# Optimization experiments

Hardware: AMD Instinct MI355X
Metric: run time of the kernel (lower is better)

The kernel has to match this reference:

```python
import jax, jax.numpy as jnp
import numpy as np

# Sizes matching init_kwargs: r=2, J=3 -> K = 1 + (r-1)*J = 4 framelet operators
N, FEAT, K, NNZ = 20000, 64, 4, 320000
NU, GAMMA, J = 2.0, 1.0, 3  # nu, gamma_0 (gamma never updated on this code path)


def setup_inputs() -> dict:
    key = jax.random.key(0)
    ks = jax.random.split(key, 6)
    F = jax.random.normal(ks[0], (N, FEAT), dtype=jnp.float32)
    w_rows = jax.random.randint(ks[1], (K, NNZ), 0, N, dtype=jnp.int32)
    w_cols = jax.random.randint(ks[2], (K, NNZ), 0, N, dtype=jnp.int32)
    # scale ~1/avg_degree so the 14-step fixed-point iteration is contractive/stable
    w_vals = jax.random.normal(ks[3], (K, NNZ), dtype=jnp.float32) / 16.0
    d = jax.random.uniform(ks[4], (N,), dtype=jnp.float32)
    mask = jax.random.uniform(ks[5], (N, 1), dtype=jnp.float32)
    return {"F": F, "w_rows": w_rows, "w_cols": w_cols, "w_vals": w_vals,
            "d": d, "mask": mask, "thres_iter": 15}


def _spmm(rows, cols, vals, X):
    # sparse [N,N] @ dense [N,FEAT] via gather + segment-sum scatter
    return jax.ops.segment_sum(vals[:, None] * X[cols], rows, num_segments=N)


_spmm_shared = jax.vmap(_spmm, in_axes=(0, 0, 0, None))  # K operators, one dense X
_spmm_each = jax.vmap(_spmm, in_axes=(0, 0, 0, 0))       # K operators, K dense Xs


def _soft(x, thr):  # elementwise soft-thresholding: relu(x-t) - relu(-x-t)
    return jax.nn.relu(x - thr) - jax.nn.relu(-x - thr)


def reference(F, w_rows, w_cols, w_vals, d, mask, thres_iter):
    # nu_jl = [0] + [nu / 4^i for i in range(J)]
    nu = jnp.asarray([0.0] + [NU / (4.0 ** i) for i in range(J)], dtype=jnp.float32)  # [K]
    thr = (nu / GAMMA)[:, None, None] * d[None, :, None]  # [K,N,1] per-operator row thresholds
    d1 = d[:, None]                 # [N,1]
    m2 = mask * mask                # [N,1]
    denom = d1 * m2 + GAMMA         # [N,1]
    num_f = d1 * F * m2             # [N,FEAT]
    Y0 = jnp.zeros((K, N, FEAT), dtype=F.dtype)

    def step(carry, _):
        Uk, Y = carry
        # Z(k+1): soft-threshold of W_jl @ Uk + Y_jl / gamma
        Z = _soft(_spmm_shared(w_rows, w_cols, w_vals, Uk) + Y / GAMMA, thr)  # [K,N,FEAT]
        v = Y - GAMMA * Z
        WTV = _spmm_each(w_rows, w_cols, w_vals, v).sum(axis=0)               # [N,FEAT]
        Uk = (num_f - WTV) / denom
        # Y(k+1) dual update
        Y = Y + GAMMA * (_spmm_shared(w_rows, w_cols, w_vals, Uk) - Z)
        return (Uk, Y), None

    n_iter = int(thres_iter) - 1  # while k < thres_iter starting at k=1
    (Uk, _), _ = jax.lax.scan(jax.checkpoint(step), (F, Y0), None, length=n_iter)
    return Uk
```

## Files before the change

kernel.cpp:

```cpp
#include <hip/hip_runtime.h>


constexpr int N_    = 20000;
constexpr int FEAT_ = 64;
constexpr int K_    = 4;
constexpr int NNZ_  = 320000;
constexpr int NF    = N_ * FEAT_;
constexpr int KN    = K_ * N_;
constexpr int NEDGE = K_ * NNZ_;
constexpr int NITER = 14;
constexpr int BLK   = 256;
constexpr int NSB   = (KN + 255) / 256;
constexpr int NCPY  = 8;
constexpr int NXCD  = 8;
constexpr int EPV   = 2048;
constexpr int NVB   = NEDGE / EPV;

constexpr int T_SP  = 3;
constexpr int NW_SP = (N_ + T_SP - 1) / T_SP;
constexpr int NB_SP4 = (NW_SP + 3) / 4;
constexpr int TABSZ = 204;

constexpr int R_WT  = 4;
constexpr int NB_WT = ((N_ + R_WT - 1) / R_WT + 3) / 4;

__constant__ float c_nu[4] = {0.0f, 2.0f, 0.5f, 0.125f};

__device__ __forceinline__ float softf(float x, float t) {
    float a = fabsf(x) - t;
    a = a > 0.0f ? a : 0.0f;
    return copysignf(a, x);
}

__device__ __forceinline__ float bf2f(unsigned short u) {
    union { unsigned int i; float f; } x;
    x.i = ((unsigned int)u) << 16;
    return x.f;
}
__device__ __forceinline__ unsigned short f2bf(float f) {
    union { float f; unsigned int i; } x;
    x.f = f;
    unsigned int r = x.i + 0x7FFFu + ((x.i >> 16) & 1u);
    return (unsigned short)(r >> 16);
}

__device__ __forceinline__ void decode_meta(unsigned int p, int& c, float& v) {
    c = (int)((p >> 15) & 3u) * N_ + (int)(p & 0x7FFFu);
    unsigned int e5 = (p >> 26) & 0x1Fu;
    unsigned int bits = (p & 0x80000000u) | ((e5 + 96u) << 23) |
                        (((p >> 17) & 0x1FFu) << 14);
    v = (e5 == 0u) ? 0.0f : __uint_as_float(bits);
}

__device__ __forceinline__ unsigned long long enc_tab(unsigned int p) {
    unsigned int c16 = (p & 0x7FFFu) << 4;
    unsigned int e5 = (p >> 26) & 0x1Fu;
    unsigned int vb = (p & 0x80000000u) | ((e5 + 96u) << 23) |
                      (((p >> 17) & 0x1FFu) << 14);
    vb = (e5 == 0u) ? 0u : vb;
    return ((unsigned long long)vb << 32) | (unsigned long long)c16;
}

__device__ __forceinline__ void fma4(float4& acc, float v, const ushort4& x) {
    acc.x += v * bf2f(x.x);
    acc.y += v * bf2f(x.y);
    acc.z += v * bf2f(x.z);
    acc.w += v * bf2f(x.w);
}


__global__ __launch_bounds__(BLK) void precompute_kernel(
    const float* __restrict__ F, const float* __restrict__ d,
    const float* __restrict__ mask, float* __restrict__ dm,
    unsigned short* __restrict__ F_bf) {
    int i = blockIdx.x * BLK + threadIdx.x;
    if (i >= NF / 4) return;
    float4 f = ((const float4*)F)[i];
    ushort4 o;
    o.x = f2bf(f.x); o.y = f2bf(f.y); o.z = f2bf(f.z); o.w = f2bf(f.w);
    ((ushort4*)F_bf)[i] = o;
    if ((i & (FEAT_ / 4 - 1)) == 0) {
        int n = i / (FEAT_ / 4);
        dm[n] = d[n] * mask[n] * mask[n];
    }
}

__global__ __launch_bounds__(BLK) void hist_kernel(
    const int* __restrict__ rows, int* __restrict__ cnt8) {
    int e = blockIdx.x * BLK + threadIdx.x;
    if (e >= NEDGE) return;
    int k = e / NNZ_;
    int copy = blockIdx.x & (NCPY - 1);
    atomicAdd(&cnt8[copy * KN + rows[e] * K_ + k], 1);
}

__global__ __launch_bounds__(256) void scan1_kernel(
    const int* __restrict__ cnt8, int* __restrict__ loc,
    int* __restrict__ bsum) {
    int i = blockIdx.x * 256 + threadIdx.x;
    int x = 0;
    if (i < KN) {
        #pragma unroll
        for (int c = 0; c < NCPY; ++c) x += cnt8[c * KN + i];
    }
    int lane = threadIdx.x & 63, wid = threadIdx.x >> 6;
    int v = x;
    #pragma unroll
    for (int off = 1; off < 64; off <<= 1) {
        int t = __shfl_up(v, off, 64);
        if (lane >= off) v += t;
    }
    __shared__ int ws[4];
    if (lane == 63) ws[wid] = v;
    __syncthreads();
    int add = 0;
    for (int u = 0; u < wid; ++u) add += ws[u];
    v += add;
    if (i < KN) loc[i] = v - x;
    if (threadIdx.x == 255) bsum[blockIdx.x] = v;
}

__global__ __launch_bounds__(512) void scan2_kernel(int* __restrict__ bsum) {
    int tid = threadIdx.x;
    int x = (tid < NSB) ? bsum[tid] : 0;
    int lane = tid & 63, wid = tid >> 6;
    int v = x;
    #pragma unroll
    for (int off = 1; off < 64; off <<= 1) {
        int t = __shfl_up(v, off, 64);
        if (lane >= off) v += t;
    }
    __shared__ int ws[8];
    if (lane == 63) ws[wid] = v;
    __syncthreads();
    int add = 0;
    for (int u = 0; u < wid; ++u) add += ws[u];
    v += add;
    if (tid < NSB) bsum[tid] = v - x;
}

__global__ __launch_bounds__(256) void scan3_kernel(
    const int* __restrict__ loc, const int* __restrict__ bsum,
    int* __restrict__ offs, int* __restrict__ cursor) {
    int i = blockIdx.x * 256 + threadIdx.x;
    if (i < KN) {
        int v = loc[i] + bsum[blockIdx.x];
        offs[i] = v;
        cursor[i] = v;
    }
    if (i == 0) offs[KN] = NEDGE;
}

__global__ __launch_bounds__(BLK) void scatter_kernel(
    const int* __restrict__ rows, const int* __restrict__ cols,
    const float* __restrict__ vals, int* __restrict__ cursor,
    unsigned int* __restrict__ cmeta) {
    int xcd = blockIdx.x & (NXCD - 1);
    int vb  = blockIdx.x >> 3;
    int ebase = vb * EPV;
    #pragma unroll
    for (int i = 0; i < EPV / BLK; ++i) {
        int e = ebase + i * BLK + threadIdx.x;
        int row = rows[e];
        if (row / (N_ / NXCD) != xcd) continue;
        int k = e / NNZ_;
        unsigned int b  = __float_as_uint(vals[e]);
        unsigned int rb = b + 0x1FFFu + ((b >> 14) & 1u);
        int exp8 = (int)((rb >> 23) & 0xFF);
        unsigned int pk = 0u;
        if (exp8 > 96)
            pk = (b & 0x80000000u) | ((unsigned int)(exp8 - 96) << 26) |
                 (((rb >> 14) & 0x1FFu) << 17);
        pk |= ((unsigned int)k << 15) | (unsigned int)cols[e];
        int pos = atomicAdd(&cursor[row * K_ + k], 1);
        cmeta[pos] = pk;
    }
}


template <int BATCH>
__device__ __forceinline__ void chunk_accum(
    int c_l, float v_l, int n, const ushort4* __restrict__ Xb,
    int sub, int q, float4& acc) {
    int iters = (n + 3) >> 2;
    int itersPad = (iters + BATCH - 1) & ~(BATCH - 1);
    for (int it0 = 0; it0 < itersPad; it0 += BATCH) {
        float   vv[BATCH];
        ushort4 xx[BATCH];
        #pragma unroll
        for (int u = 0; u < BATCH; ++u) {
            int j = 4 * (it0 + u) + sub;
            int   c = __shfl(c_l, j, 64);
            vv[u]   = __shfl(v_l, j, 64);
            xx[u]   = Xb[c * (FEAT_ / 4) + q];
        }
        #pragma unroll
        for (int u = 0; u < BATCH; ++u) {
            acc.x += vv[u] * bf2f(xx[u].x);
            acc.y += vv[u] * bf2f(xx[u].y);
            acc.z += vv[u] * bf2f(xx[u].z);
            acc.w += vv[u] * bf2f(xx[u].w);
        }
    }
}

template <int BATCH>
__device__ __forceinline__ void tail_accum(
    const unsigned int* __restrict__ cmeta, const ushort4* __restrict__ Xb,
    int beg, int end, int lane, int sub, int q, int padc, float4& acc) {
    for (int eb = beg; eb < end; eb += 64) {
        int n = end - eb;
        if (n > 64) n = 64;
        int   c_l = padc;
        float v_l = 0.0f;
        if (lane < n) {
            unsigned int p = cmeta[eb + lane];
            decode_meta(p, c_l, v_l);
        }
        chunk_accum<BATCH>(c_l, v_l, n, Xb, sub, q, acc);
    }
}

__device__ __forceinline__ void butterfly4(float4& a) {
    #pragma unroll
    for (int m = 16; m <= 32; m <<= 1) {
        a.x += __shfl_xor(a.x, m, 64);
        a.y += __shfl_xor(a.y, m, 64);
        a.z += __shfl_xor(a.z, m, 64);
        a.w += __shfl_xor(a.w, m, 64);
    }
}

template <bool FIRST>
__global__ __launch_bounds__(BLK) void spmm_fused_kernel(
    const int* __restrict__ offs, const unsigned int* __restrict__ cmeta,
    const unsigned short* __restrict__ Xb,
    const float* __restrict__ d, unsigned short* __restrict__ V_bf) {
    __shared__ unsigned long long tab[4][2][TABSZ];
    int wave = (blockIdx.x * BLK + threadIdx.x) >> 6;
    int lane = threadIdx.x & 63;
    int sub  = lane >> 4, q = lane & 15;
    int widx = threadIdx.x >> 6;
    int n0 = wave * T_SP;
    if (n0 >= N_) return;
    int off_l = 0;
    if (lane <= 4 * T_SP) {
        int i = n0 * K_ + lane;
        if (i > KN) i = KN;
        off_l = offs[i];
    }
    const ushort4* X4 = (const ushort4*)Xb;
    ushort4* V4 = (ushort4*)V_bf;
    float nu_s = sub == 0 ? 0.0f : (sub == 1 ? 2.0f : (sub == 2 ? 0.5f : 0.125f));

    int tb = __shfl(off_l, 0, 64);
    int te = __shfl(off_l, 4, 64);
    int span = te - tb;
    unsigned int pA = 0, pB = 0, pC = 0;
    if (lane < span)       pA = cmeta[tb + lane];
    if (64 + lane < span)  pB = cmeta[tb + 64 + lane];
    if (128 + lane < span) pC = cmeta[tb + 128 + lane];

    #pragma unroll
    for (int t = 0; t < T_SP; ++t) {
        int n = n0 + t;
        if (n >= N_) break;
        unsigned long long* Tc = tab[widx][t & 1];
        int bs = __shfl(off_l, 4 * t + sub, 64);
        int es = __shfl(off_l, 4 * t + sub + 1, 64);
        int pre = bs - tb;
        int cnt = es - bs;
        int jmax = 192 - pre;
        jmax = cnt < jmax ? cnt : jmax;
        if (jmax < 0) jmax = 0;
        int maxc = jmax;
        { int o1 = __shfl_xor(maxc, 16, 64); maxc = maxc > o1 ? maxc : o1;
          int o2 = __shfl_xor(maxc, 32, 64); maxc = maxc > o2 ? maxc : o2; }
        if (lane < span)       { int s = lane;       Tc[s + (s >> 4)] = enc_tab(pA); }
        if (64 + lane < span)  { int s = 64 + lane;  Tc[s + (s >> 4)] = enc_tab(pB); }
        if (128 + lane < span) { int s = 128 + lane; Tc[s + (s >> 4)] = enc_tab(pC); }
        int tbn = te, ten = te, spann = 0;
        unsigned int nA = 0, nB = 0, nC = 0;
        if (t + 1 < T_SP && n + 1 < N_) {
            ten = __shfl(off_l, 4 * t + 8, 64);
            spann = ten - tbn;
            if (lane < spann)       nA = cmeta[tbn + lane];
            if (64 + lane < spann)  nB = cmeta[tbn + 64 + lane];
            if (128 + lane < spann) nC = cmeta[tbn + 128 + lane];
        }
        asm volatile("s_waitcnt lgkmcnt(0)" ::: "memory");
        float4 acc = {0.f, 0.f, 0.f, 0.f};
        for (int i0 = 0; i0 < maxc; i0 += 4) {
            float vv[4]; int cc[4];
            #pragma unroll
            for (int u = 0; u < 4; ++u) {
                int j = i0 + u;
                bool ok = j < jmax;
                int slot = ok ? pre + j : 0;
                unsigned long long e = Tc[slot + (slot >> 4)];
                cc[u] = (int)(unsigned int)e;
                vv[u] = ok ? __uint_as_float((unsigned int)(e >> 32)) : 0.0f;
            }
            ushort4 xx[4];
            #pragma unroll
            for (int u = 0; u < 4; ++u) xx[u] = X4[cc[u] + q];
            #pragma unroll
            for (int u = 0; u < 4; ++u) fma4(acc, vv[u], xx[u]);
        }
        if (span > 192) {
            for (int e = tb + 192; e < te; ++e) {
                unsigned int p = cmeta[e];
                int ke = (int)((p >> 15) & 3u);
                unsigned long long en = enc_tab(p);
                if (sub == ke) {
                    ushort4 x = X4[(int)(unsigned int)en + q];
                    fma4(acc, __uint_as_float((unsigned int)(en >> 32)), x);
                }
            }
        }
        {
            float dn = d[n];
            int idx4 = (sub * N_ + n) * (FEAT_ / 4) + q;
            float thr = nu_s * dn;
            float4 y;
            if (FIRST) {
                y = make_float4(0.f, 0.f, 0.f, 0.f);
            } else {
                ushort4 vp = V4[idx4];
                y.x = acc.x + bf2f(vp.x); y.y = acc.y + bf2f(vp.y);
                y.z = acc.z + bf2f(vp.z); y.w = acc.w + bf2f(vp.w);
            }
            ushort4 o;
            o.x = f2bf(y.x - softf(acc.x + y.x, thr));
            o.y = f2bf(y.y - softf(acc.y + y.y, thr));
            o.z = f2bf(y.z - softf(acc.z + y.z, thr));
            o.w = f2bf(y.w - softf(acc.w + y.w, thr));
            V4[idx4] = o;
        }
        tb = tbn; te = ten; span = spann;
        pA = nA; pB = nB; pC = nC;
    }
}

template <bool LAST>
__global__ __launch_bounds__(BLK) void wtv_u_kernel(
    const int* __restrict__ offs, const unsigned int* __restrict__ cmeta,
    const unsigned short* __restrict__ V_bf,
    const float* __restrict__ F, const float* __restrict__ dm,
    float* __restrict__ U, unsigned short* __restrict__ U_bf) {
    int wave = (blockIdx.x * BLK + threadIdx.x) >> 6;
    int lane = threadIdx.x & 63;
    int sub  = lane >> 4, q = lane & 15;
    int base = wave * R_WT;
    if (base >= N_) return;
    int off_l = 0;
    if (lane <= K_ * R_WT) {
        int i = K_ * base + lane;
        if (i > KN) i = KN;
        off_l = offs[i];
    }
    const ushort4* V4 = (const ushort4*)V_bf;

    unsigned int p0 = 0u, p1 = 0u;
    {
        int b0 = __shfl(off_l, 0, 64), e0 = __shfl(off_l, K_, 64);
        int nn = e0 - b0;
        if (lane < nn) p0 = cmeta[b0 + lane];
        if (64 + lane < nn) p1 = cmeta[b0 + 64 + lane];
    }
    for (int r = 0; r < R_WT; ++r) {
        int n = base + r;
        if (n >= N_) break;
        int beg = __shfl(off_l, K_ * r, 64);
        int end = __shfl(off_l, K_ * r + K_, 64);
        unsigned int q0 = 0u, q1 = 0u;
        if (r + 1 < R_WT && n + 1 < N_) {
            int bn = __shfl(off_l, K_ * r + K_, 64);
            int en = __shfl(off_l, K_ * r + 2 * K_, 64);
            int nn = en - bn;
            if (lane < nn) q0 = cmeta[bn + lane];
            if (64 + lane < nn) q1 = cmeta[bn + 64 + lane];
        }
        int ne = end - beg;
        float4 acc = {0.f, 0.f, 0.f, 0.f};
        {
            int n0c = ne > 64 ? 64 : ne;
            int   c_l = 0;
            float v_l = 0.0f;
            if (lane < n0c) decode_meta(p0, c_l, v_l);
            chunk_accum<8>(c_l, v_l, n0c, V4, sub, q, acc);
        }
        if (ne > 64) {
            int n1 = ne - 64;
            if (n1 > 64) n1 = 64;
            int   c_l = 0;
            float v_l = 0.0f;
            if (lane < n1) decode_meta(p1, c_l, v_l);
            chunk_accum<2>(c_l, v_l, n1, V4, sub, q, acc);
        }
        if (ne > 128)
            tail_accum<2>(cmeta, V4, beg + 128, end, lane, sub, q, 0, acc);
        p0 = q0; p1 = q1;
        butterfly4(acc);
        if (sub == 0) {
            int idx4 = n * (FEAT_ / 4) + q;
            float dmv = dm[n];
            float r2 = 1.0f / (dmv + 1.0f);
            float4 f = ((const float4*)F)[idx4];
            float4 o;
            o.x = (dmv * f.x - acc.x) * r2; o.y = (dmv * f.y - acc.y) * r2;
            o.z = (dmv * f.z - acc.z) * r2; o.w = (dmv * f.w - acc.w) * r2;
            if (LAST) ((float4*)U)[idx4] = o;
            ushort4 ob;
            ob.x = f2bf(o.x); ob.y = f2bf(o.y);
            ob.z = f2bf(o.z); ob.w = f2bf(o.w);
            ((ushort4*)U_bf)[idx4] = ob;
        }
    }
}

extern "C" void kernel_launch(void* const* d_in, const int* in_sizes, int n_in,
                              void* d_out, int out_size, void* d_ws, size_t ws_size,
                              hipStream_t stream) {
    const float* F      = (const float*)d_in[0];
    const int*   w_rows = (const int*)d_in[1];
    const int*   w_cols = (const int*)d_in[2];
    const float* w_vals = (const float*)d_in[3];
    const float* d      = (const float*)d_in[4];
    const float* mask   = (const float*)d_in[5];
    float* U = (float*)d_out;

    unsigned int* cmeta  = (unsigned int*)d_ws;
    unsigned short* V_bf = (unsigned short*)(cmeta + NEDGE);
    unsigned short* U_bf = V_bf + (size_t)KN * FEAT_;
    unsigned short* F_bf = U_bf + NF;
    float* dm     = (float*)(F_bf + NF);
    int*   cnt8   = (int*)(dm + N_);
    int*   loc    = cnt8 + NCPY * KN;
    int*   bsum   = loc + KN;
    int*   offs   = bsum + 512;
    int*   cursor = offs + KN + 1;

    const int gEdge = NEDGE / BLK;
    const int gNF4  = (NF / 4) / BLK;

    hipMemsetAsync(cnt8, 0, (size_t)NCPY * KN * 4, stream);
    precompute_kernel<<<gNF4, BLK, 0, stream>>>(F, d, mask, dm, F_bf);
    hist_kernel<<<gEdge, BLK, 0, stream>>>(w_rows, cnt8);
    scan1_kernel<<<NSB, 256, 0, stream>>>(cnt8, loc, bsum);
    scan2_kernel<<<1, 512, 0, stream>>>(bsum);
    scan3_kernel<<<NSB, 256, 0, stream>>>(loc, bsum, offs, cursor);
    scatter_kernel<<<NVB * NXCD, BLK, 0, stream>>>(w_rows, w_cols, w_vals,
                                                   cursor, cmeta);

    spmm_fused_kernel<true><<<NB_SP4, BLK, 0, stream>>>(offs, cmeta, F_bf, d, V_bf);
    for (int it = 0; it < NITER; ++it) {
        if (it < NITER - 1) {
            wtv_u_kernel<false><<<NB_WT, BLK, 0, stream>>>(offs, cmeta, V_bf,
                                                           F, dm, U, U_bf);
            spmm_fused_kernel<false><<<NB_SP4, BLK, 0, stream>>>(offs, cmeta,
                                                                 U_bf, d, V_bf);
        } else {
            wtv_u_kernel<true><<<NB_WT, BLK, 0, stream>>>(offs, cmeta, V_bf,
                                                          F, dm, U, U_bf);
        }
    }
}
```

Measured before the change: 817.5 us.

## Restructure WTV kernel: one row per 16-lane group with LDS-staged edge table

After: 788.2 us. -3.6%, faster.

```diff
diff --git a/kernel.cpp b/kernel.cpp
--- a/kernel.cpp
+++ b/kernel.cpp
@@ -21,8 +21,9 @@
 constexpr int NB_SP4 = (NW_SP + 3) / 4;
 constexpr int TABSZ = 204;
 
-constexpr int R_WT  = 4;
-constexpr int NB_WT = ((N_ + R_WT - 1) / R_WT + 3) / 4;
+constexpr int NB_WT4 = ((N_ / 4) + 3) / 4;
+constexpr int WCAP  = 384;
+constexpr int TABW  = WCAP + WCAP / 16;
 
 __constant__ float c_nu[4] = {0.0f, 2.0f, 0.5f, 0.125f};
 
@@ -44,21 +45,22 @@
     return (unsigned short)(r >> 16);
 }
 
-__device__ __forceinline__ void decode_meta(unsigned int p, int& c, float& v) {
-    c = (int)((p >> 15) & 3u) * N_ + (int)(p & 0x7FFFu);
-    unsigned int e5 = (p >> 26) & 0x1Fu;
-    unsigned int bits = (p & 0x80000000u) | ((e5 + 96u) << 23) |
-                        (((p >> 17) & 0x1FFu) << 14);
-    v = (e5 == 0u) ? 0.0f : __uint_as_float(bits);
-}
-
-__device__ __forceinline__ unsigned long long enc_tab(unsigned int p) {
-    unsigned int c16 = (p & 0x7FFFu) << 4;
+__device__ __forceinline__ unsigned int val_bits(unsigned int p) {
     unsigned int e5 = (p >> 26) & 0x1Fu;
     unsigned int vb = (p & 0x80000000u) | ((e5 + 96u) << 23) |
                       (((p >> 17) & 0x1FFu) << 14);
-    vb = (e5 == 0u) ? 0u : vb;
-    return ((unsigned long long)vb << 32) | (unsigned long long)c16;
+    return (e5 == 0u) ? 0u : vb;
+}
+
+__device__ __forceinline__ unsigned long long enc_tab(unsigned int p) {
+    unsigned int c16 = (p & 0x7FFFu) << 4;
+    return ((unsigned long long)val_bits(p) << 32) | (unsigned long long)c16;
+}
+
+__device__ __forceinline__ unsigned long long enc_wtv(unsigned int p) {
+    unsigned int c16 = (((p >> 15) & 3u) * (unsigned int)N_ +
+                        (p & 0x7FFFu)) << 4;
+    return ((unsigned long long)val_bits(p) << 32) | (unsigned long long)c16;
 }
 
 __device__ __forceinline__ void fma4(float4& acc, float v, const ushort4& x) {
@@ -177,59 +179,6 @@
     }
 }
 
-
-template <int BATCH>
-__device__ __forceinline__ void chunk_accum(
-    int c_l, float v_l, int n, const ushort4* __restrict__ Xb,
-    int sub, int q, float4& acc) {
-    int iters = (n + 3) >> 2;
-    int itersPad = (iters + BATCH - 1) & ~(BATCH - 1);
-    for (int it0 = 0; it0 < itersPad; it0 += BATCH) {
-        float   vv[BATCH];
-        ushort4 xx[BATCH];
-        #pragma unroll
-        for (int u = 0; u < BATCH; ++u) {
-            int j = 4 * (it0 + u) + sub;
-            int   c = __shfl(c_l, j, 64);
-            vv[u]   = __shfl(v_l, j, 64);
-            xx[u]   = Xb[c * (FEAT_ / 4) + q];
-        }
-        #pragma unroll
-        for (int u = 0; u < BATCH; ++u) {
-            acc.x += vv[u] * bf2f(xx[u].x);
-            acc.y += vv[u] * bf2f(xx[u].y);
-            acc.z += vv[u] * bf2f(xx[u].z);
-            acc.w += vv[u] * bf2f(xx[u].w);
-        }
-    }
-}
-
-template <int BATCH>
-__device__ __forceinline__ void tail_accum(
-    const unsigned int* __restrict__ cmeta, const ushort4* __restrict__ Xb,
-    int beg, int end, int lane, int sub, int q, int padc, float4& acc) {
-    for (int eb = beg; eb < end; eb += 64) {
-        int n = end - eb;
-        if (n > 64) n = 64;
-        int   c_l = padc;
-        float v_l = 0.0f;
-        if (lane < n) {
-            unsigned int p = cmeta[eb + lane];
-            decode_meta(p, c_l, v_l);
-        }
-        chunk_accum<BATCH>(c_l, v_l, n, Xb, sub, q, acc);
-    }
-}
-
-__device__ __forceinline__ void butterfly4(float4& a) {
-    #pragma unroll
-    for (int m = 16; m <= 32; m <<= 1) {
-        a.x += __shfl_xor(a.x, m, 64);
-        a.y += __shfl_xor(a.y, m, 64);
-        a.z += __shfl_xor(a.z, m, 64);
-        a.w += __shfl_xor(a.w, m, 64);
-    }
-}
 
 template <bool FIRST>
 __global__ __launch_bounds__(BLK) void spmm_fused_kernel(
@@ -348,74 +297,89 @@
     const unsigned short* __restrict__ V_bf,
     const float* __restrict__ F, const float* __restrict__ dm,
     float* __restrict__ U, unsigned short* __restrict__ U_bf) {
+    __shared__ unsigned long long tab[4][TABW];
     int wave = (blockIdx.x * BLK + threadIdx.x) >> 6;
     int lane = threadIdx.x & 63;
     int sub  = lane >> 4, q = lane & 15;
-    int base = wave * R_WT;
-    if (base >= N_) return;
+    int widx = threadIdx.x >> 6;
+    int n0 = wave * 4;
+    if (n0 >= N_) return;
     int off_l = 0;
-    if (lane <= K_ * R_WT) {
-        int i = K_ * base + lane;
+    if (lane <= 16) {
+        int i = n0 * K_ + lane;
         if (i > KN) i = KN;
         off_l = offs[i];
     }
     const ushort4* V4 = (const ushort4*)V_bf;
 
-    unsigned int p0 = 0u, p1 = 0u;
+    int tb = __shfl(off_l, 0, 64);
+    int te = __shfl(off_l, 16, 64);
+    int span = te - tb;
+    unsigned int pr[6];
+    #pragma unroll
+    for (int c = 0; c < 6; ++c) {
+        pr[c] = 0u;
+        if (c * 64 + lane < span) pr[c] = cmeta[tb + c * 64 + lane];
+    }
+    int bs = __shfl(off_l, 4 * sub, 64);
+    int es = __shfl(off_l, 4 * sub + 4, 64);
+    int pre = bs - tb;
+    int cnt = es - bs;
+    int jmax = WCAP - pre;
+    jmax = cnt < jmax ? cnt : jmax;
+    if (jmax < 0) jmax = 0;
+    int maxc = jmax;
+    { int o1 = __shfl_xor(maxc, 16, 64); maxc = maxc > o1 ? maxc : o1;
+      int o2 = __shfl_xor(maxc, 32, 64); maxc = maxc > o2 ? maxc : o2; }
+    unsigned long long* Tc = tab[widx];
+    #pragma unroll
+    for (int c = 0; c < 6; ++c) {
+        int s = c * 64 + lane;
+        if (s < span) Tc[s + (s >> 4)] = enc_wtv(pr[c]);
+    }
+    asm volatile("s_waitcnt lgkmcnt(0)" ::: "memory");
+    float4 acc = {0.f, 0.f, 0.f, 0.f};
+    for (int i0 = 0; i0 < maxc; i0 += 4) {
+        float vv[4]; int cc[4];
+        #pragma unroll
+        for (int u = 0; u < 4; ++u) {
+            int j = i0 + u;
+            bool ok = j < jmax;
+            int slot = ok ? pre + j : 0;
+            unsigned long long e = Tc[slot + (slot >> 4)];
+            cc[u] = (int)(unsigned int)e;
+            vv[u] = ok ? __uint_as_float((unsigned int)(e >> 32)) : 0.0f;
+        }
+        ushort4 xx[4];
+        #pragma unroll
+        for (int u = 0; u < 4; ++u) xx[u] = V4[cc[u] + q];
+        #pragma unroll
+        for (int u = 0; u < 4; ++u) fma4(acc, vv[u], xx[u]);
+    }
+    if (span > WCAP) {
+        for (int e = tb + WCAP; e < te; ++e) {
+            unsigned int p = cmeta[e];
+            unsigned long long en = enc_wtv(p);
+            if (e >= bs && e < es) {
+                ushort4 x = V4[(int)(unsigned int)en + q];
+                fma4(acc, __uint_as_float((unsigned int)(en >> 32)), x);
+            }
+        }
+    }
     {
-        int b0 = __shfl(off_l, 0, 64), e0 = __shfl(off_l, K_, 64);
-        int nn = e0 - b0;
-        if (lane < nn) p0 = cmeta[b0 + lane];
-        if (64 + lane < nn) p1 = cmeta[b0 + 64 + lane];
-    }
-    for (int r = 0; r < R_WT; ++r) {
-        int n = base + r;
-        if (n >= N_) break;
-        int beg = __shfl(off_l, K_ * r, 64);
-        int end = __shfl(off_l, K_ * r + K_, 64);
-        unsigned int q0 = 0u, q1 = 0u;
-        if (r + 1 < R_WT && n + 1 < N_) {
-            int bn = __shfl(off_l, K_ * r + K_, 64);
-            int en = __shfl(off_l, K_ * r + 2 * K_, 64);
-            int nn = en - bn;
-            if (lane < nn) q0 = cmeta[bn + lane];
-            if (64 + lane < nn) q1 = cmeta[bn + 64 + lane];
-        }
-        int ne = end - beg;
-        float4 acc = {0.f, 0.f, 0.f, 0.f};
-        {
-            int n0c = ne > 64 ? 64 : ne;
-            int   c_l = 0;
-            float v_l = 0.0f;
-            if (lane < n0c) decode_meta(p0, c_l, v_l);
-            chunk_accum<8>(c_l, v_l, n0c, V4, sub, q, acc);
-        }
-        if (ne > 64) {
-            int n1 = ne - 64;
-            if (n1 > 64) n1 = 64;
-            int   c_l = 0;
-            float v_l = 0.0f;
-            if (lane < n1) decode_meta(p1, c_l, v_l);
-            chunk_accum<2>(c_l, v_l, n1, V4, sub, q, acc);
-        }
-        if (ne > 128)
-            tail_accum<2>(cmeta, V4, beg + 128, end, lane, sub, q, 0, acc);
-        p0 = q0; p1 = q1;
-        butterfly4(acc);
-        if (sub == 0) {
-            int idx4 = n * (FEAT_ / 4) + q;
-            float dmv = dm[n];
-            float r2 = 1.0f / (dmv + 1.0f);
-            float4 f = ((const float4*)F)[idx4];
-            float4 o;
-            o.x = (dmv * f.x - acc.x) * r2; o.y = (dmv * f.y - acc.y) * r2;
-            o.z = (dmv * f.z - acc.z) * r2; o.w = (dmv * f.w - acc.w) * r2;
-            if (LAST) ((float4*)U)[idx4] = o;
-            ushort4 ob;
-            ob.x = f2bf(o.x); ob.y = f2bf(o.y);
-            ob.z = f2bf(o.z); ob.w = f2bf(o.w);
-            ((ushort4*)U_bf)[idx4] = ob;
-        }
+        int n = n0 + sub;
+        float dmv = dm[n];
+        float r2 = 1.0f / (dmv + 1.0f);
+        int idx4 = n * (FEAT_ / 4) + q;
+        float4 f = ((const float4*)F)[idx4];
+        float4 o;
+        o.x = (dmv * f.x - acc.x) * r2; o.y = (dmv * f.y - acc.y) * r2;
+        o.z = (dmv * f.z - acc.z) * r2; o.w = (dmv * f.w - acc.w) * r2;
+        if (LAST) ((float4*)U)[idx4] = o;
+        ushort4 ob;
+        ob.x = f2bf(o.x); ob.y = f2bf(o.y);
+        ob.z = f2bf(o.z); ob.w = f2bf(o.w);
+        ((ushort4*)U_bf)[idx4] = ob;
     }
 }
 
@@ -456,13 +420,13 @@
     spmm_fused_kernel<true><<<NB_SP4, BLK, 0, stream>>>(offs, cmeta, F_bf, d, V_bf);
     for (int it = 0; it < NITER; ++it) {
         if (it < NITER - 1) {
-            wtv_u_kernel<false><<<NB_WT, BLK, 0, stream>>>(offs, cmeta, V_bf,
-                                                           F, dm, U, U_bf);
+            wtv_u_kernel<false><<<NB_WT4, BLK, 0, stream>>>(offs, cmeta, V_bf,
+                                                            F, dm, U, U_bf);
             spmm_fused_kernel<false><<<NB_SP4, BLK, 0, stream>>>(offs, cmeta,
                                                                  U_bf, d, V_bf);
         } else {
-            wtv_u_kernel<true><<<NB_WT, BLK, 0, stream>>>(offs, cmeta, V_bf,
-                                                          F, dm, U, U_bf);
-        }
-    }
-}
+            wtv_u_kernel<true><<<NB_WT4, BLK, 0, stream>>>(offs, cmeta, V_bf,
+                                                           F, dm, U, U_bf);
+        }
+    }
+}
```
